# Kernel optimization log

Hardware: AMD Instinct MI355X
Metric: run time of the kernel (lower is better)

## Reference

```python
import jax, jax.numpy as jnp
import numpy as np

N = 100000
E = 1600000
F_DIM = 128
H_DIM = 64
K_CLUSTERS = 16
NEG_SLOPE = 0.2


def setup_inputs() -> dict:
    key = jax.random.key(0)
    ks = jax.random.split(key, 10)
    X = jax.random.normal(ks[0], (N, F_DIM), dtype=jnp.float32)
    ei_feat = jax.random.randint(ks[1], (2, E), 0, N, dtype=jnp.int64)
    batch = jnp.zeros((N,), dtype=jnp.int64)
    # GATv2Conv layer 1 params (heads=1): lin_l, lin_r [F,H], att [H], bias [H]
    s1 = 1.0 / np.sqrt(F_DIM)
    W1l = jax.random.uniform(ks[2], (F_DIM, H_DIM), jnp.float32, -s1, s1)
    W1r = jax.random.uniform(ks[3], (F_DIM, H_DIM), jnp.float32, -s1, s1)
    a1 = jax.random.uniform(ks[4], (H_DIM,), jnp.float32, -1/np.sqrt(H_DIM), 1/np.sqrt(H_DIM))
    b1 = jnp.zeros((H_DIM,), jnp.float32)
    # layer 2: [H,K]
    s2 = 1.0 / np.sqrt(H_DIM)
    W2l = jax.random.uniform(ks[5], (H_DIM, K_CLUSTERS), jnp.float32, -s2, s2)
    W2r = jax.random.uniform(ks[6], (H_DIM, K_CLUSTERS), jnp.float32, -s2, s2)
    a2 = jax.random.uniform(ks[7], (K_CLUSTERS,), jnp.float32, -1/np.sqrt(K_CLUSTERS), 1/np.sqrt(K_CLUSTERS))
    b2 = jnp.zeros((K_CLUSTERS,), jnp.float32)
    return {"X": X, "ei_feat": ei_feat, "batch": batch,
            "W1l": W1l, "W1r": W1r, "a1": a1, "b1": b1,
            "W2l": W2l, "W2r": W2r, "a2": a2, "b2": b2}


def gatv2_conv(x, src, dst, Wl, Wr, a, b, n_nodes):
    # GATv2 (heads=1): e_ij = a^T LeakyReLU(Wl x_j + Wr x_i); softmax over j->i; out_i = sum alpha * Wl x_j
    xl = x @ Wl            # [N,H] source transform
    xr = x @ Wr            # [N,H] target transform
    e = jax.nn.leaky_relu(xl[src] + xr[dst], NEG_SLOPE) @ a   # [E']
    m = jax.ops.segment_max(e, dst, num_segments=n_nodes)      # stable softmax per target
    w = jnp.exp(e - m[dst])
    denom = jax.ops.segment_sum(w, dst, num_segments=n_nodes)
    alpha = w / denom[dst]  # every node has a self-loop, so denom > 0
    out = jax.ops.segment_sum(alpha[:, None] * xl[src], dst, num_segments=n_nodes)
    return out + b


def reference(X, ei_feat, batch, W1l, W1r, a1, b1, W2l, W2r, a2, b2):
    loop = jnp.arange(N, dtype=ei_feat.dtype)
    src = jnp.concatenate([ei_feat[0], loop])  # add_self_loops=True (PyG default)
    dst = jnp.concatenate([ei_feat[1], loop])
    h = jax.nn.elu(gatv2_conv(X, src, dst, W1l, W1r, a1, b1, N))
    z = gatv2_conv(h, src, dst, W2l, W2r, a2, b2, N)
    return jax.nn.softmax(z, axis=1)
```

## Files before the change

kernel.cpp:

```cpp
#include <hip/hip_runtime.h>
#include <stdint.h>

#define F_DIM 128
#define H_DIM 64
#define K_DIM 16
#define BUK_SH 8
#define NCH 256

typedef _Float16 half2v __attribute__((ext_vector_type(2)));
typedef _Float16 half4 __attribute__((ext_vector_type(4)));
typedef _Float16 f16x8 __attribute__((ext_vector_type(8)));
typedef float f32x4 __attribute__((ext_vector_type(4)));

__device__ __forceinline__ void gload_lds16(const void* g, void* l) {
    __builtin_amdgcn_global_load_lds(
        (const __attribute__((address_space(1))) void*)g,
        (__attribute__((address_space(3))) void*)l, 16, 0, 0);
}

__global__ __launch_bounds__(256) void k_hist(const int* __restrict__ dst,
                                              int* __restrict__ hist,
                                              int E, int CH, int NBUK) {
    __shared__ int h[512];
    int t = threadIdx.x, c = blockIdx.x;
    for (int i = t; i < NBUK; i += 256) h[i] = 0;
    __syncthreads();
    int s = c * CH, e = min(s + CH, E);
    for (int i = s + t; i < e; i += 256) atomicAdd(&h[dst[i] >> BUK_SH], 1);
    __syncthreads();
    for (int i = t; i < NBUK; i += 256) hist[i * NCH + c] = h[i];
}

__global__ __launch_bounds__(256) void k_scanBkt(int* __restrict__ hist,
                                                 int* __restrict__ bktTot) {
    __shared__ int sh[256];
    int b = blockIdx.x, t = threadIdx.x;
    int v = hist[b * NCH + t];
    sh[t] = v;
    __syncthreads();
    for (int off = 1; off < 256; off <<= 1) {
        int x = (t >= off) ? sh[t - off] : 0;
        __syncthreads();
        sh[t] += x;
        __syncthreads();
    }
    hist[b * NCH + t] = sh[t] - v;
    if (t == 255) bktTot[b] = sh[255];
}

__global__ __launch_bounds__(256) void k_scanTot(const int* __restrict__ bktTot,
                                                 int* __restrict__ bktBase, int NBUK) {
    __shared__ int sh[256];
    int t = threadIdx.x;
    int i0 = 2 * t, i1 = 2 * t + 1;
    int v0 = (i0 < NBUK) ? bktTot[i0] : 0;
    int v1 = (i1 < NBUK) ? bktTot[i1] : 0;
    int s = v0 + v1;
    sh[t] = s;
    __syncthreads();
    for (int off = 1; off < 256; off <<= 1) {
        int x = (t >= off) ? sh[t - off] : 0;
        __syncthreads();
        sh[t] += x;
        __syncthreads();
    }
    int excl = sh[t] - s;
    if (i0 < NBUK) bktBase[i0] = excl;
    if (i1 < NBUK) bktBase[i1] = excl + v0;
    if (t == 255) bktBase[NBUK] = sh[255];
}

__global__ __launch_bounds__(256) void k_scatter(const int* __restrict__ src,
                                                 const int* __restrict__ dst,
                                                 const int* __restrict__ hist,
                                                 const int* __restrict__ bktBase,
                                                 uint32_t* __restrict__ binned,
                                                 int E, int CH, int NBUK) {
    __shared__ int ctr[512];
    int t = threadIdx.x, c = blockIdx.x;
    for (int i = t; i < NBUK; i += 256) ctr[i] = bktBase[i] + hist[i * NCH + c];
    __syncthreads();
    int s = c * CH, e = min(s + CH, E);
    for (int i = s + t; i < e; i += 256) {
        int d = dst[i];
        int pos = atomicAdd(&ctr[d >> BUK_SH], 1);
        binned[pos] = (uint32_t)src[i] | ((uint32_t)(d & 255) << 20);
    }
}

__global__ __launch_bounds__(256) void k_fine2(const uint32_t* __restrict__ binned,
                                               const int* __restrict__ bktBase,
                                               int* __restrict__ rowptr,
                                               int* __restrict__ col, int N) {
    __shared__ int h[256], sc[256], slotL[256];
    int b = blockIdx.x, t = threadIdx.x;
    int n0 = b << BUK_SH;
    int s = bktBase[b], e = bktBase[b + 1];
    h[t] = 0;
    __syncthreads();
    for (int i = s + t; i < e; i += 256) atomicAdd(&h[binned[i] >> 20], 1);
    __syncthreads();
    int v = h[t];
    sc[t] = v;
    __syncthreads();
    for (int off = 1; off < 256; off <<= 1) {
        int x = (t >= off) ? sc[t - off] : 0;
        __syncthreads();
        sc[t] += x;
        __syncthreads();
    }
    int excl = sc[t] - v;
    int n = n0 + t;
    int rowbase = s + n0;
    if (n < N) {
        int rp = rowbase + excl + t;
        rowptr[n] = rp;
        col[rp] = n;
        slotL[t] = rp + 1;
        if (n == N - 1) rowptr[N] = rp + v + 1;
    }
    __syncthreads();
    for (int i = s + t; i < e; i += 256) {
        uint32_t p = binned[i];
        int pos = atomicAdd(&slotL[p >> 20], 1);
        col[pos] = (int)(p & 0xFFFFFu);
    }
}

__global__ __launch_bounds__(256) void k_swzW(const float* __restrict__ W1l,
                                              const float* __restrict__ W1r,
                                              const float* __restrict__ W2l,
                                              const float* __restrict__ W2r,
                                              _Float16* __restrict__ Wg1,
                                              _Float16* __restrict__ Wg2) {
    int t = threadIdx.x;
    if (blockIdx.x == 0) {
        for (int i = t; i < 4096; i += 256) {
            int k = i >> 5, c4 = (i & 31) << 2;
            float4 v = (c4 < 64) ? *(const float4*)&W1l[k * 64 + c4]
                                 : *(const float4*)&W1r[k * 64 + (c4 - 64)];
            int s = k >> 5, q = (k >> 3) & 3, j = k & 7;
            float vv[4] = {v.x, v.y, v.z, v.w};
#pragma unroll
            for (int u = 0; u < 4; ++u) {
                int C = c4 + u, c = C >> 4, n = C & 15;
                Wg1[(((c * 4 + s) * 4 + q) * 16 + n) * 8 + j] = (_Float16)vv[u];
            }
        }
    } else {
        for (int i = t; i < 512; i += 256) {
            int k = i >> 3, c4 = (i & 7) << 2;
            float4 v = (c4 < 16) ? *(const float4*)&W2l[k * 16 + c4]
                                 : *(const float4*)&W2r[k * 16 + (c4 - 16)];
            int s = k >> 5, q = (k >> 3) & 3, j = k & 7;
            float vv[4] = {v.x, v.y, v.z, v.w};
#pragma unroll
            for (int u = 0; u < 4; ++u) {
                int C = c4 + u, c = C >> 4, n = C & 15;
                Wg2[(((c * 2 + s) * 4 + q) * 16 + n) * 8 + j] = (_Float16)vv[u];
            }
        }
    }
}

__global__ __launch_bounds__(256, 4) void k_gemm1m(
        const float* __restrict__ X, const _Float16* __restrict__ Wg,
        _Float16* __restrict__ xlh, _Float16* __restrict__ xrh, int N) {
    __shared__ _Float16 Ws[16384];
    int t = threadIdx.x;
    int n0 = blockIdx.x * 32;
    int w = t >> 6, lane = t & 63, m = lane & 15, q = lane >> 4;
    int rowHalf = w >> 1, cHalf = w & 1;
    {
        int base = w * 64;
#pragma unroll
        for (int i = 0; i < 8; ++i) {
            int ch = i * 256 + base;
            gload_lds16(&Wg[(long)(ch + lane) * 8], &Ws[(long)ch * 8]);
        }
    }
    int r0 = n0 + rowHalf * 16 + m;
    int rc = (r0 < N) ? r0 : (N - 1);
    const float* p0 = X + (long)rc * 128 + q * 8;
    float4 xf[8];
#pragma unroll
    for (int s = 0; s < 4; ++s) {
        xf[2 * s]     = *(const float4*)(p0 + s * 32);
        xf[2 * s + 1] = *(const float4*)(p0 + s * 32 + 4);
    }
    f16x8 af[4];
#pragma unroll
    for (int s = 0; s < 4; ++s) {
        af[s][0] = (_Float16)xf[2 * s].x;     af[s][1] = (_Float16)xf[2 * s].y;
        af[s][2] = (_Float16)xf[2 * s].z;     af[s][3] = (_Float16)xf[2 * s].w;
        af[s][4] = (_Float16)xf[2 * s + 1].x; af[s][5] = (_Float16)xf[2 * s + 1].y;
        af[s][6] = (_Float16)xf[2 * s + 1].z; af[s][7] = (_Float16)xf[2 * s + 1].w;
    }
    __syncthreads();
    f32x4 acc[4];
#pragma unroll
    for (int c = 0; c < 4; ++c) acc[c] = (f32x4){0.f, 0.f, 0.f, 0.f};
#pragma unroll
    for (int s = 0; s < 4; ++s)
#pragma unroll
        for (int c = 0; c < 4; ++c) {
            int cc = cHalf * 4 + c;
            f16x8 b = *(const f16x8*)&Ws[(((cc * 4 + s) * 4 + q) * 16 + m) * 8];
            acc[c] = __builtin_amdgcn_mfma_f32_16x16x32_f16(af[s], b, acc[c], 0, 0, 0);
        }
    __syncthreads();
    _Float16* Tw = &Ws[w * 2048];
#pragma unroll
    for (int c = 0; c < 4; ++c)
#pragma unroll
        for (int r = 0; r < 4; ++r)
            Tw[(q * 4 + r) * 76 + c * 16 + m] = (_Float16)acc[c][r];
#pragma unroll
    for (int p = 0; p < 2; ++p) {
        int lr = p * 8 + (lane >> 3);
        int chk = lane & 7;
        f16x8 v = *(const f16x8*)&Tw[lr * 76 + chk * 8];
        int gn = n0 + rowHalf * 16 + lr;
        if (gn < N) {
            if (cHalf == 0) *(f16x8*)&xlh[(long)gn * 64 + chk * 8] = v;
            else            *(f16x8*)&xrh[(long)gn * 64 + chk * 8] = v;
        }
    }
}

__global__ __launch_bounds__(256, 4) void k_gemm2m(
        const _Float16* __restrict__ Hm, const _Float16* __restrict__ Wg2,
        _Float16* __restrict__ xlh, _Float16* __restrict__ xrh, int N) {
    __shared__ _Float16 Ws2[1024];
    __shared__ _Float16 T[4][32 * 40];
    int t = threadIdx.x;
    int n0 = blockIdx.x * 128;
    int w = t >> 6, lane = t & 63, m = lane & 15, q = lane >> 4;
    if (t < 128) *(f16x8*)&Ws2[t * 8] = *(const f16x8*)&Wg2[t * 8];
    const f16x8 zh = {0, 0, 0, 0, 0, 0, 0, 0};
    f16x8 a[2][2];
#pragma unroll
    for (int sub = 0; sub < 2; ++sub) {
        int row = n0 + w * 32 + sub * 16 + m;
        bool vr = row < N;
#pragma unroll
        for (int s = 0; s < 2; ++s)
            a[sub][s] = vr ? *(const f16x8*)&Hm[(long)row * 64 + s * 32 + q * 8] : zh;
    }
    __syncthreads();
    f32x4 acc[2][2];
#pragma unroll
    for (int sub = 0; sub < 2; ++sub)
#pragma unroll
        for (int c = 0; c < 2; ++c) acc[sub][c] = (f32x4){0.f, 0.f, 0.f, 0.f};
#pragma unroll
    for (int s = 0; s < 2; ++s)
#pragma unroll
        for (int c = 0; c < 2; ++c) {
            f16x8 b = *(const f16x8*)&Ws2[(((c * 2 + s) * 4 + q) * 16 + m) * 8];
#pragma unroll
            for (int sub = 0; sub < 2; ++sub)
                acc[sub][c] = __builtin_amdgcn_mfma_f32_16x16x32_f16(a[sub][s], b, acc[sub][c], 0, 0, 0);
        }
    _Float16* Tw = T[w];
#pragma unroll
    for (int sub = 0; sub < 2; ++sub)
#pragma unroll
    for (int c = 0; c < 2; ++c)
#pragma unroll
    for (int r = 0; r < 4; ++r)
        Tw[(sub * 16 + q * 4 + r) * 40 + c * 16 + m] = (_Float16)acc[sub][c][r];
    int lr = lane >> 1;
    int gn = n0 + w * 32 + lr;
#pragma unroll
    for (int p = 0; p < 2; ++p) {
        int cc = p * 2 + (lane & 1);
        f16x8 v = *(const f16x8*)&Tw[lr * 40 + cc * 8];
        if (gn < N) {
            if (cc < 2) *(f16x8*)&xlh[(long)gn * 16 + cc * 8] = v;
            else        *(f16x8*)&xrh[(long)gn * 16 + (cc - 2) * 8] = v;
        }
    }
}

__global__ void k_att1(const f16x8* __restrict__ xlh, const f16x8* __restrict__ xrh,
                       const float* __restrict__ a1, const float* __restrict__ b1,
                       const int* __restrict__ rowptr, const int* __restrict__ col,
                       f16x8* __restrict__ hout, int N) {
    int n = (int)((blockIdx.x * (unsigned)blockDim.x + threadIdx.x) >> 4);
    int lane = threadIdx.x & 63;
    if (n >= N) return;
    int q = lane & 7;
    int g = (lane >> 3) & 1;
    float4 af0 = ((const float4*)a1)[q * 2 + 0];
    float4 af1 = ((const float4*)a1)[q * 2 + 1];
    half2v a01 = {(_Float16)af0.x, (_Float16)af0.y};
    half2v a23 = {(_Float16)af0.z, (_Float16)af0.w};
    half2v a45 = {(_Float16)af1.x, (_Float16)af1.y};
    half2v a67 = {(_Float16)af1.z, (_Float16)af1.w};
    f16x8 xrv = xrh[(long)n * 8 + q];
    int jb = rowptr[n], je = rowptr[n + 1];
    int j0 = jb + g, jlast = je - 1;
    int d = je - jb - g;
    int T = (d > 0) ? ((d + 1) >> 1) : 0;
    float l = 0.f;
    float o[8] = {0.f, 0.f, 0.f, 0.f, 0.f, 0.f, 0.f, 0.f};
    auto jidx = [&](int k) { int j = j0 + 2 * k; return (j < jlast) ? j : jlast; };
    auto edge = [&](const f16x8& xh) {
        f16x8 t = xh + xrv;
        f16x8 u = __builtin_elementwise_max(t, t * (_Float16)0.2f);
        half2v ua = {u[0], u[1]}, ub = {u[2], u[3]}, uc = {u[4], u[5]}, ud = {u[6], u[7]};
        float e = __builtin_amdgcn_fdot2(ua, a01,
                   __builtin_amdgcn_fdot2(ub, a23,
                    __builtin_amdgcn_fdot2(uc, a45,
                     __builtin_amdgcn_fdot2(ud, a67, 0.f, false), false), false), false);
#pragma unroll
        for (int off = 1; off < 8; off <<= 1) e += __shfl_xor(e, off, 8);
        float c = __expf(e);
        l += c;
#pragma unroll
        for (int i = 0; i < 8; ++i) o[i] = fmaf(c, (float)xh[i], o[i]);
    };
    f16x8 xA = xlh[(long)col[jidx(0)] * 8 + q];
    f16x8 xB = xlh[(long)col[jidx(1)] * 8 + q];
    int cA = col[jidx(2)];
    int cB = col[jidx(3)];
    int k = 0;
    for (; k + 2 <= T; k += 2) {
        int cA2 = col[jidx(k + 4)];
        int cB2 = col[jidx(k + 5)];
        edge(xA);
        xA = xlh[(long)cA * 8 + q];
        edge(xB);
        xB = xlh[(long)cB * 8 + q];
        cA = cA2; cB = cB2;
    }
    if (k < T) edge(xA);
    l += __shfl_xor(l, 8);
#pragma unroll
    for (int i = 0; i < 8; ++i) o[i] += __shfl_xor(o[i], 8);
    if (g == 0) {
        float4 bv0 = ((const float4*)b1)[q * 2 + 0];
        float4 bv1 = ((const float4*)b1)[q * 2 + 1];
        float bb[8] = {bv0.x, bv0.y, bv0.z, bv0.w, bv1.x, bv1.y, bv1.z, bv1.w};
        float rl = 1.f / l;
        f16x8 hv;
#pragma unroll
        for (int i = 0; i < 8; ++i) {
            float h = o[i] * rl + bb[i];
            h = (h > 0.f) ? h : (__expf(h) - 1.f);
            hv[i] = (_Float16)h;
        }
        hout[(long)n * 8 + q] = hv;
    }
}

__global__ void k_att2(const half4* __restrict__ xlh, const half4* __restrict__ xrh,
                       const float* __restrict__ a2, const float* __restrict__ b2v,
                       const int* __restrict__ rowptr, const int* __restrict__ col,
                       float* __restrict__ out, int N) {
    int n = (int)((blockIdx.x * (unsigned)blockDim.x + threadIdx.x) >> 4);
    int lane = threadIdx.x & 63;
    if (n >= N) return;
    int q = lane & 3;
    int g = (lane >> 2) & 3;
    float4 af = ((const float4*)a2)[q];
    half2v alo = {(_Float16)af.x, (_Float16)af.y};
    half2v ahi = {(_Float16)af.z, (_Float16)af.w};
    half4 xrv = xrh[(long)n * 4 + q];
    int jb = rowptr[n], je = rowptr[n + 1];
    int j0 = jb + g, jlast = je - 1;
    int d = je - jb - g;
    int T = (d > 0) ? ((d + 3) >> 2) : 0;
    float l = 0.f;
    float4 o = {0.f, 0.f, 0.f, 0.f};
    auto jidx = [&](int k) { int j = j0 + 4 * k; return (j < jlast) ? j : jlast; };
    auto edge = [&](const half4& xh) {
        half4 t = xh + xrv;
        half4 u = __builtin_elementwise_max(t, t * (_Float16)0.2f);
        half2v ulo = {u.x, u.y}, uhi = {u.z, u.w};
        float e = __builtin_amdgcn_fdot2(ulo, alo,
                   __builtin_amdgcn_fdot2(uhi, ahi, 0.f, false), false);
        e += __shfl_xor(e, 1, 4);
        e += __shfl_xor(e, 2, 4);
        float c = __expf(e);
        l += c;
        o.x = fmaf(c, (float)xh.x, o.x);
        o.y = fmaf(c, (float)xh.y, o.y);
        o.z = fmaf(c, (float)xh.z, o.z);
        o.w = fmaf(c, (float)xh.w, o.w);
    };
    half4 xA = xlh[(long)col[jidx(0)] * 4 + q];
    half4 xB = xlh[(long)col[jidx(1)] * 4 + q];
    int cA = col[jidx(2)];
    int cB = col[jidx(3)];
    int k = 0;
    for (; k + 2 <= T; k += 2) {
        int cA2 = col[jidx(k + 4)];
        int cB2 = col[jidx(k + 5)];
        edge(xA);
        xA = xlh[(long)cA * 4 + q];
        edge(xB);
        xB = xlh[(long)cB * 4 + q];
        cA = cA2; cB = cB2;
    }
    if (k < T) edge(xA);
#pragma unroll
    for (int off = 4; off <= 8; off <<= 1) {
        l   += __shfl_xor(l, off);
        o.x += __shfl_xor(o.x, off);
        o.y += __shfl_xor(o.y, off);
        o.z += __shfl_xor(o.z, off);
        o.w += __shfl_xor(o.w, off);
    }
    if (g == 0) {
        float4 bv = ((const float4*)b2v)[q];
        float rl = 1.f / l;
        float4 z;
        z.x = o.x * rl + bv.x;
        z.y = o.y * rl + bv.y;
        z.z = o.z * rl + bv.z;
        z.w = o.w * rl + bv.w;
        float mx = fmaxf(fmaxf(z.x, z.y), fmaxf(z.z, z.w));
        mx = fmaxf(mx, __shfl_xor(mx, 1, 4));
        mx = fmaxf(mx, __shfl_xor(mx, 2, 4));
        float4 ez;
        ez.x = __expf(z.x - mx); ez.y = __expf(z.y - mx);
        ez.z = __expf(z.z - mx); ez.w = __expf(z.w - mx);
        float ss = ez.x + ez.y + ez.z + ez.w;
        ss += __shfl_xor(ss, 1, 4);
        ss += __shfl_xor(ss, 2, 4);
        float rs = 1.f / ss;
        ez.x *= rs; ez.y *= rs; ez.z *= rs; ez.w *= rs;
        ((float4*)out)[(long)n * 4 + q] = ez;
    }
}

extern "C" void kernel_launch(void* const* d_in, const int* in_sizes, int n_in,
                              void* d_out, int out_size, void* d_ws, size_t ws_size,
                              hipStream_t stream) {
    const float* X   = (const float*)d_in[0];
    const int*   ei  = (const int*)d_in[1];
    const float* W1l = (const float*)d_in[3];
    const float* W1r = (const float*)d_in[4];
    const float* a1  = (const float*)d_in[5];
    const float* b1  = (const float*)d_in[6];
    const float* W2l = (const float*)d_in[7];
    const float* W2r = (const float*)d_in[8];
    const float* a2  = (const float*)d_in[9];
    const float* b2  = (const float*)d_in[10];

    int N = in_sizes[0] / F_DIM;
    int E = in_sizes[1] / 2;
    int M = E + N;
    int NBUK = (N + 255) >> BUK_SH;
    int NH = NBUK * NCH;
    int CH = (E + NCH - 1) / NCH;
    const int* srcv = ei;
    const int* dstv = ei + E;

    char* w = (char*)d_ws;
    size_t off = 0;
    auto alloc = [&](size_t bytes) -> char* {
        char* p = w + off;
        off = (off + bytes + 255) & ~(size_t)255;
        return p;
    };
    int* rowptr  = (int*)alloc((size_t)(N + 1) * sizeof(int));
    int* hist    = (int*)alloc((size_t)NH * sizeof(int));
    int* bktTot  = (int*)alloc((size_t)NBUK * sizeof(int));
    int* bktBase = (int*)alloc((size_t)(NBUK + 1) * sizeof(int));
    int* col     = (int*)alloc((size_t)M * sizeof(int));
    uint32_t* binned = (uint32_t*)alloc((size_t)E * sizeof(uint32_t));
    _Float16* xl1h = (_Float16*)alloc((size_t)N * H_DIM * 2);
    _Float16* xr1h = (_Float16*)alloc((size_t)N * H_DIM * 2);
    _Float16* h1h  = (_Float16*)alloc((size_t)N * H_DIM * 2);
    _Float16* xl2h = (_Float16*)alloc((size_t)N * K_DIM * 2);
    _Float16* xr2h = (_Float16*)alloc((size_t)N * K_DIM * 2);
    _Float16* Wg1  = (_Float16*)alloc((size_t)16384 * 2);
    _Float16* Wg2  = (_Float16*)alloc((size_t)2048 * 2);

    k_swzW<<<2, 256, 0, stream>>>(W1l, W1r, W2l, W2r, Wg1, Wg2);
    k_hist<<<NCH, 256, 0, stream>>>(dstv, hist, E, CH, NBUK);
    k_scanBkt<<<NBUK, 256, 0, stream>>>(hist, bktTot);
    k_scanTot<<<1, 256, 0, stream>>>(bktTot, bktBase, NBUK);
    k_scatter<<<NCH, 256, 0, stream>>>(srcv, dstv, hist, bktBase, binned, E, CH, NBUK);
    k_fine2<<<NBUK, 256, 0, stream>>>(binned, bktBase, rowptr, col, N);

    int g1Blocks = (N + 31) / 32;
    k_gemm1m<<<g1Blocks, 256, 0, stream>>>(X, Wg1, xl1h, xr1h, N);
    int nodeBlocks16 = (N + 15) / 16;
    k_att1<<<nodeBlocks16, 256, 0, stream>>>((const f16x8*)xl1h, (const f16x8*)xr1h,
                                             a1, b1, rowptr, col, (f16x8*)h1h, N);
    int g2Blocks = (N + 127) / 128;
    k_gemm2m<<<g2Blocks, 256, 0, stream>>>(h1h, Wg2, xl2h, xr2h, N);
    k_att2<<<nodeBlocks16, 256, 0, stream>>>((const half4*)xl2h, (const half4*)xr2h,
                                             a2, b2, rowptr, col, (float*)d_out, N);
}
```

Before: 237.4 us.

## Replace bucketed two-pass CSR build with global-atomic degree count and scatter

The CSR construction moves from a two-level bucketed histogram/scatter in LDS to a direct approach: a global-atomic per-node degree count, a two-level block scan, row finalisation, and a scatter that places each edge with a global atomicAdd on its node's cursor. This drops the intermediate binned array and the second fine-grained pass, cutting memory traffic and kernel count. In exchange it relies on many contended global atomics across 100k counters and makes the column order inside each row nondeterministic, which can change floating-point summation order.

New measurement: 379.7 us. +60.0%, slower.

```diff
diff --git a/kernel.cpp b/kernel.cpp
--- a/kernel.cpp
+++ b/kernel.cpp
@@ -4,8 +4,6 @@
 #define F_DIM 128
 #define H_DIM 64
 #define K_DIM 16
-#define BUK_SH 8
-#define NCH 256
 
 typedef _Float16 half2v __attribute__((ext_vector_type(2)));
 typedef _Float16 half4 __attribute__((ext_vector_type(4)));
@@ -18,24 +16,19 @@
         (__attribute__((address_space(3))) void*)l, 16, 0, 0);
 }
 
-__global__ __launch_bounds__(256) void k_hist(const int* __restrict__ dst,
-                                              int* __restrict__ hist,
-                                              int E, int CH, int NBUK) {
-    __shared__ int h[512];
-    int t = threadIdx.x, c = blockIdx.x;
-    for (int i = t; i < NBUK; i += 256) h[i] = 0;
-    __syncthreads();
-    int s = c * CH, e = min(s + CH, E);
-    for (int i = s + t; i < e; i += 256) atomicAdd(&h[dst[i] >> BUK_SH], 1);
-    __syncthreads();
-    for (int i = t; i < NBUK; i += 256) hist[i * NCH + c] = h[i];
-}
-
-__global__ __launch_bounds__(256) void k_scanBkt(int* __restrict__ hist,
-                                                 int* __restrict__ bktTot) {
+__global__ __launch_bounds__(256) void k_deg(const int* __restrict__ dst,
+                                             int* __restrict__ cnt, int E) {
+    int i = blockIdx.x * 256 + threadIdx.x;
+    int stride = gridDim.x * 256;
+    for (; i < E; i += stride) atomicAdd(&cnt[dst[i]], 1);
+}
+
+__global__ __launch_bounds__(256) void k_scanA(const int* __restrict__ cnt,
+                                               int* __restrict__ rowtmp,
+                                               int* __restrict__ blockTot, int N) {
     __shared__ int sh[256];
-    int b = blockIdx.x, t = threadIdx.x;
-    int v = hist[b * NCH + t];
+    int b = blockIdx.x, t = threadIdx.x, n = b * 256 + t;
+    int v = (n < N) ? cnt[n] : 0;
     sh[t] = v;
     __syncthreads();
     for (int off = 1; off < 256; off <<= 1) {
@@ -44,8 +37,8 @@
         sh[t] += x;
         __syncthreads();
     }
-    hist[b * NCH + t] = sh[t] - v;
-    if (t == 255) bktTot[b] = sh[255];
+    if (n < N) rowtmp[n] = sh[t] - v;
+    if (t == 255) blockTot[b] = sh[255];
 }
 
 __global__ __launch_bounds__(256) void k_scanTot(const int* __restrict__ bktTot,
@@ -70,60 +63,30 @@
     if (t == 255) bktBase[NBUK] = sh[255];
 }
 
-__global__ __launch_bounds__(256) void k_scatter(const int* __restrict__ src,
-                                                 const int* __restrict__ dst,
-                                                 const int* __restrict__ hist,
-                                                 const int* __restrict__ bktBase,
-                                                 uint32_t* __restrict__ binned,
-                                                 int E, int CH, int NBUK) {
-    __shared__ int ctr[512];
-    int t = threadIdx.x, c = blockIdx.x;
-    for (int i = t; i < NBUK; i += 256) ctr[i] = bktBase[i] + hist[i * NCH + c];
-    __syncthreads();
-    int s = c * CH, e = min(s + CH, E);
-    for (int i = s + t; i < e; i += 256) {
-        int d = dst[i];
-        int pos = atomicAdd(&ctr[d >> BUK_SH], 1);
-        binned[pos] = (uint32_t)src[i] | ((uint32_t)(d & 255) << 20);
-    }
-}
-
-__global__ __launch_bounds__(256) void k_fine2(const uint32_t* __restrict__ binned,
-                                               const int* __restrict__ bktBase,
-                                               int* __restrict__ rowptr,
-                                               int* __restrict__ col, int N) {
-    __shared__ int h[256], sc[256], slotL[256];
-    int b = blockIdx.x, t = threadIdx.x;
-    int n0 = b << BUK_SH;
-    int s = bktBase[b], e = bktBase[b + 1];
-    h[t] = 0;
-    __syncthreads();
-    for (int i = s + t; i < e; i += 256) atomicAdd(&h[binned[i] >> 20], 1);
-    __syncthreads();
-    int v = h[t];
-    sc[t] = v;
-    __syncthreads();
-    for (int off = 1; off < 256; off <<= 1) {
-        int x = (t >= off) ? sc[t - off] : 0;
-        __syncthreads();
-        sc[t] += x;
-        __syncthreads();
-    }
-    int excl = sc[t] - v;
-    int n = n0 + t;
-    int rowbase = s + n0;
+__global__ __launch_bounds__(256) void k_fin(const int* __restrict__ rowtmp,
+                                             const int* __restrict__ blockBase,
+                                             int* __restrict__ rowptr,
+                                             int* __restrict__ col,
+                                             int* __restrict__ cnt, int N, int M) {
+    int n = blockIdx.x * 256 + threadIdx.x;
     if (n < N) {
-        int rp = rowbase + excl + t;
-        rowptr[n] = rp;
-        col[rp] = n;
-        slotL[t] = rp + 1;
-        if (n == N - 1) rowptr[N] = rp + v + 1;
-    }
-    __syncthreads();
-    for (int i = s + t; i < e; i += 256) {
-        uint32_t p = binned[i];
-        int pos = atomicAdd(&slotL[p >> 20], 1);
-        col[pos] = (int)(p & 0xFFFFFu);
+        int base = blockBase[blockIdx.x] + rowtmp[n] + n;
+        rowptr[n] = base;
+        col[base] = n;
+        cnt[n] = base + 1;
+        if (n == N - 1) rowptr[N] = M;
+    }
+}
+
+__global__ __launch_bounds__(256) void k_scat(const int* __restrict__ src,
+                                              const int* __restrict__ dst,
+                                              int* __restrict__ cnt,
+                                              int* __restrict__ col, int E) {
+    int i = blockIdx.x * 256 + threadIdx.x;
+    int stride = gridDim.x * 256;
+    for (; i < E; i += stride) {
+        int pos = atomicAdd(&cnt[dst[i]], 1);
+        col[pos] = src[i];
     }
 }
 
@@ -453,9 +416,7 @@
     int N = in_sizes[0] / F_DIM;
     int E = in_sizes[1] / 2;
     int M = E + N;
-    int NBUK = (N + 255) >> BUK_SH;
-    int NH = NBUK * NCH;
-    int CH = (E + NCH - 1) / NCH;
+    int NBLK = (N + 255) >> 8;
     const int* srcv = ei;
     const int* dstv = ei + E;
 
@@ -466,12 +427,12 @@
         off = (off + bytes + 255) & ~(size_t)255;
         return p;
     };
-    int* rowptr  = (int*)alloc((size_t)(N + 1) * sizeof(int));
-    int* hist    = (int*)alloc((size_t)NH * sizeof(int));
-    int* bktTot  = (int*)alloc((size_t)NBUK * sizeof(int));
-    int* bktBase = (int*)alloc((size_t)(NBUK + 1) * sizeof(int));
-    int* col     = (int*)alloc((size_t)M * sizeof(int));
-    uint32_t* binned = (uint32_t*)alloc((size_t)E * sizeof(uint32_t));
+    int* rowptr   = (int*)alloc((size_t)(N + 1) * sizeof(int));
+    int* cnt      = (int*)alloc((size_t)N * sizeof(int));
+    int* rowtmp   = (int*)alloc((size_t)N * sizeof(int));
+    int* blockTot = (int*)alloc((size_t)NBLK * sizeof(int));
+    int* blockBase= (int*)alloc((size_t)(NBLK + 1) * sizeof(int));
+    int* col      = (int*)alloc((size_t)M * sizeof(int));
     _Float16* xl1h = (_Float16*)alloc((size_t)N * H_DIM * 2);
     _Float16* xr1h = (_Float16*)alloc((size_t)N * H_DIM * 2);
     _Float16* h1h  = (_Float16*)alloc((size_t)N * H_DIM * 2);
@@ -481,11 +442,13 @@
     _Float16* Wg2  = (_Float16*)alloc((size_t)2048 * 2);
 
     k_swzW<<<2, 256, 0, stream>>>(W1l, W1r, W2l, W2r, Wg1, Wg2);
-    k_hist<<<NCH, 256, 0, stream>>>(dstv, hist, E, CH, NBUK);
-    k_scanBkt<<<NBUK, 256, 0, stream>>>(hist, bktTot);
-    k_scanTot<<<1, 256, 0, stream>>>(bktTot, bktBase, NBUK);
-    k_scatter<<<NCH, 256, 0, stream>>>(srcv, dstv, hist, bktBase, binned, E, CH, NBUK);
-    k_fine2<<<NBUK, 256, 0, stream>>>(binned, bktBase, rowptr, col, N);
+    hipMemsetAsync(cnt, 0, (size_t)N * sizeof(int), stream);
+    int egrid = 2048;
+    k_deg<<<egrid, 256, 0, stream>>>(dstv, cnt, E);
+    k_scanA<<<NBLK, 256, 0, stream>>>(cnt, rowtmp, blockTot, N);
+    k_scanTot<<<1, 256, 0, stream>>>(blockTot, blockBase, NBLK);
+    k_fin<<<NBLK, 256, 0, stream>>>(rowtmp, blockBase, rowptr, col, cnt, N, M);
+    k_scat<<<egrid, 256, 0, stream>>>(srcv, dstv, cnt, col, E);
 
     int g1Blocks = (N + 31) / 32;
     k_gemm1m<<<g1Blocks, 256, 0, stream>>>(X, Wg1, xl1h, xr1h, N);
```

## Sort nodes by in-degree so attention wavefronts process similar-degree nodes

Applied to the files above, without the earlier changes.

Adds a counting sort of nodes by in-degree (capped at 63) using a histogram, the existing scan kernels, and a scatter into a permutation array. Both attention kernels now pick their node through this permutation, so the nodes sharing a wavefront have similar edge counts and lanes wait less on the longest row. The cost is four extra small kernel launches, an extra indirection per node, and scattered output writes and row reads in place of contiguous ones.

Measured after the change: 250.7 us. 5.6% more time.

```diff
diff --git a/kernel.cpp b/kernel.cpp
--- a/kernel.cpp
+++ b/kernel.cpp
@@ -124,6 +124,39 @@
         uint32_t p = binned[i];
         int pos = atomicAdd(&slotL[p >> 20], 1);
         col[pos] = (int)(p & 0xFFFFFu);
+    }
+}
+
+__global__ __launch_bounds__(256) void k_dhist(const int* __restrict__ rowptr,
+                                               int* __restrict__ dh, int N, int CHN) {
+    __shared__ int h[64];
+    int t = threadIdx.x, c = blockIdx.x;
+    if (t < 64) h[t] = 0;
+    __syncthreads();
+    int s = c * CHN, e = min(s + CHN, N);
+    for (int i = s + t; i < e; i += 256) {
+        int d = rowptr[i + 1] - rowptr[i];
+        d = (d > 63) ? 63 : d;
+        atomicAdd(&h[d], 1);
+    }
+    __syncthreads();
+    if (t < 64) dh[t * NCH + c] = h[t];
+}
+
+__global__ __launch_bounds__(256) void k_dscat(const int* __restrict__ rowptr,
+                                               const int* __restrict__ dh,
+                                               const int* __restrict__ dBase,
+                                               int* __restrict__ perm, int N, int CHN) {
+    __shared__ int ctr[64];
+    int t = threadIdx.x, c = blockIdx.x;
+    if (t < 64) ctr[t] = dBase[t] + dh[t * NCH + c];
+    __syncthreads();
+    int s = c * CHN, e = min(s + CHN, N);
+    for (int i = s + t; i < e; i += 256) {
+        int d = rowptr[i + 1] - rowptr[i];
+        d = (d > 63) ? 63 : d;
+        int pos = atomicAdd(&ctr[d], 1);
+        perm[pos] = i;
     }
 }
 
@@ -286,10 +319,12 @@
 __global__ void k_att1(const f16x8* __restrict__ xlh, const f16x8* __restrict__ xrh,
                        const float* __restrict__ a1, const float* __restrict__ b1,
                        const int* __restrict__ rowptr, const int* __restrict__ col,
+                       const int* __restrict__ perm,
                        f16x8* __restrict__ hout, int N) {
-    int n = (int)((blockIdx.x * (unsigned)blockDim.x + threadIdx.x) >> 4);
+    int slot = (int)((blockIdx.x * (unsigned)blockDim.x + threadIdx.x) >> 4);
     int lane = threadIdx.x & 63;
-    if (n >= N) return;
+    if (slot >= N) return;
+    int n = perm[slot];
     int q = lane & 7;
     int g = (lane >> 3) & 1;
     float4 af0 = ((const float4*)a1)[q * 2 + 0];
@@ -358,10 +393,12 @@
 __global__ void k_att2(const half4* __restrict__ xlh, const half4* __restrict__ xrh,
                        const float* __restrict__ a2, const float* __restrict__ b2v,
                        const int* __restrict__ rowptr, const int* __restrict__ col,
+                       const int* __restrict__ perm,
                        float* __restrict__ out, int N) {
-    int n = (int)((blockIdx.x * (unsigned)blockDim.x + threadIdx.x) >> 4);
+    int slot = (int)((blockIdx.x * (unsigned)blockDim.x + threadIdx.x) >> 4);
     int lane = threadIdx.x & 63;
-    if (n >= N) return;
+    if (slot >= N) return;
+    int n = perm[slot];
     int q = lane & 3;
     int g = (lane >> 2) & 3;
     float4 af = ((const float4*)a2)[q];
@@ -456,6 +493,7 @@
     int NBUK = (N + 255) >> BUK_SH;
     int NH = NBUK * NCH;
     int CH = (E + NCH - 1) / NCH;
+    int CHN = (N + NCH - 1) / NCH;
     const int* srcv = ei;
     const int* dstv = ei + E;
 
@@ -472,6 +510,10 @@
     int* bktBase = (int*)alloc((size_t)(NBUK + 1) * sizeof(int));
     int* col     = (int*)alloc((size_t)M * sizeof(int));
     uint32_t* binned = (uint32_t*)alloc((size_t)E * sizeof(uint32_t));
+    int* dh      = (int*)alloc((size_t)64 * NCH * sizeof(int));
+    int* dTot    = (int*)alloc((size_t)64 * sizeof(int));
+    int* dBase   = (int*)alloc((size_t)65 * sizeof(int));
+    int* perm    = (int*)alloc((size_t)N * sizeof(int));
     _Float16* xl1h = (_Float16*)alloc((size_t)N * H_DIM * 2);
     _Float16* xr1h = (_Float16*)alloc((size_t)N * H_DIM * 2);
     _Float16* h1h  = (_Float16*)alloc((size_t)N * H_DIM * 2);
@@ -487,13 +529,18 @@
     k_scatter<<<NCH, 256, 0, stream>>>(srcv, dstv, hist, bktBase, binned, E, CH, NBUK);
     k_fine2<<<NBUK, 256, 0, stream>>>(binned, bktBase, rowptr, col, N);
 
+    k_dhist<<<NCH, 256, 0, stream>>>(rowptr, dh, N, CHN);
+    k_scanBkt<<<64, 256, 0, stream>>>(dh, dTot);
+    k_scanTot<<<1, 256, 0, stream>>>(dTot, dBase, 64);
+    k_dscat<<<NCH, 256, 0, stream>>>(rowptr, dh, dBase, perm, N, CHN);
+
     int g1Blocks = (N + 31) / 32;
     k_gemm1m<<<g1Blocks, 256, 0, stream>>>(X, Wg1, xl1h, xr1h, N);
     int nodeBlocks16 = (N + 15) / 16;
     k_att1<<<nodeBlocks16, 256, 0, stream>>>((const f16x8*)xl1h, (const f16x8*)xr1h,
-                                             a1, b1, rowptr, col, (f16x8*)h1h, N);
+                                             a1, b1, rowptr, col, perm, (f16x8*)h1h, N);
     int g2Blocks = (N + 127) / 128;
     k_gemm2m<<<g2Blocks, 256, 0, stream>>>(h1h, Wg2, xl2h, xr2h, N);
     k_att2<<<nodeBlocks16, 256, 0, stream>>>((const half4*)xl2h, (const half4*)xr2h,
-                                             a2, b2, rowptr, col, (float*)d_out, N);
-}
+                                             a2, b2, rowptr, col, perm, (float*)d_out, N);
+}
```
